# Performance work log

Measured on AMD Instinct MI355X. Metric: run time of the kernel, lower is better.

The kernel has to match this reference:

```python
import jax, jax.numpy as jnp
import numpy as np

NUM_WIRES = 20
DEPTH = 4


def setup_inputs() -> dict:
    key = jax.random.key(0)
    x = jax.random.normal(key, (NUM_WIRES,), dtype=jnp.float32)
    return {"x": x}


def _apply_1q(state, gate, wire):
    # state: flat [2^n] complex; apply 2x2 gate on `wire`
    s = state.reshape(2 ** wire, 2, -1)
    return jnp.einsum('ab,ibj->iaj', gate, s).reshape(-1)


def _apply_cnot(state, control):
    # CNOT on adjacent wires (control, control+1): flip target where control==1
    s = state.reshape(2 ** control, 2, 2, -1)
    s = jnp.concatenate([s[:, :1], s[:, 1:, ::-1]], axis=1)
    return s.reshape(-1)


def _simulate(x):
    n = NUM_WIRES
    state = jnp.zeros(2 ** n, dtype=jnp.complex64).at[0].set(1.0)
    half = (x.astype(jnp.float32) * 0.5)
    c = jnp.cos(half).astype(jnp.complex64)  # [n]
    s = jnp.sin(half).astype(jnp.complex64)  # [n]
    for _ in range(DEPTH):
        for w in range(n):
            cw, sw = c[w], s[w]
            rx = jnp.stack([jnp.stack([cw, -1j * sw]), jnp.stack([-1j * sw, cw])])
            ry = jnp.stack([jnp.stack([cw, -sw]), jnp.stack([sw, cw])])
            state = _apply_1q(state, rx, w)
            state = _apply_1q(state, ry, w)
        for w in range(n - 1):
            state = _apply_cnot(state, w)
    probs = jnp.abs(state) ** 2  # real float32 [2^n]
    expz = []
    for i in range(n):
        p = probs.reshape(2 ** i, 2, -1).sum(axis=(0, 2))
        expz.append(p[0] - p[1])
    return jnp.stack(expz).astype(jnp.float32)  # [n] <Z_i>


def reference(x):
    return _simulate(x)
```

## Files before the change

kernel.cpp:

```cpp
#include <hip/hip_runtime.h>


#define NW 20

__device__ __forceinline__ float2 cmul(float2 a, float2 b) {
    return make_float2(a.x*b.x - a.y*b.y, a.x*b.y + a.y*b.x);
}

__device__ __forceinline__ void apply_gate(float2& a0, float2& a1,
                                           float2 u00, float2 u01,
                                           float2 u10, float2 u11) {
    float2 b0, b1;
    b0.x = u00.x*a0.x - u00.y*a0.y + u01.x*a1.x - u01.y*a1.y;
    b0.y = u00.x*a0.y + u00.y*a0.x + u01.x*a1.y + u01.y*a1.x;
    b1.x = u10.x*a0.x - u10.y*a0.y + u11.x*a1.x - u11.y*a1.y;
    b1.y = u10.x*a0.y + u10.y*a0.x + u11.x*a1.y + u11.y*a1.x;
    a0 = b0; a1 = b1;
}

__device__ __forceinline__ float2 shflx(float2 v, int m) {
    float2 r;
    r.x = __shfl_xor(v.x, m, 64);
    r.y = __shfl_xor(v.y, m, 64);
    return r;
}

template<int A>
__device__ __forceinline__ void gate_regbit(float2 (&amp)[8], const float2* __restrict__ Gw) {
    float2 u00 = Gw[0], u01 = Gw[1], u10 = Gw[2], u11 = Gw[3];
    #pragma unroll
    for (int r = 0; r < 8; r++)
        if (!(r & (1 << A)))
            apply_gate(amp[r], amp[r | (1 << A)], u00, u01, u10, u11);
}

template<int A, int LM>
__device__ __forceinline__ void swap_reg_lane(float2 (&amp)[8], unsigned lane) {
    bool hb = (lane & (unsigned)LM) != 0u;
    #pragma unroll
    for (int r = 0; r < 8; r++) {
        if (!(r & (1 << A))) {
            float2 lo = amp[r], hi = amp[r | (1 << A)];
            float2 xs = hb ? lo : hi;
            float2 ys = shflx(xs, LM);
            amp[r]            = hb ? ys : lo;
            amp[r | (1 << A)] = hb ? hi : ys;
        }
    }
}

__global__ void prep_gates(const float* __restrict__ x, float2* __restrict__ G) {
    int w = threadIdx.x;
    if (w < NW) {
        float h = 0.5f * x[w];
        float c = cosf(h), s = sinf(h);
        float cc = c*c, ss = s*s, cs = c*s;
        G[w*4+0] = make_float2(cc,  ss);
        G[w*4+1] = make_float2(-cs, -cs);
        G[w*4+2] = make_float2(cs,  -cs);
        G[w*4+3] = make_float2(cc,  -ss);
    }
}

template<int MODE>
__global__ __launch_bounds__(512) void stageA(const float2* __restrict__ src,
                                              float2* __restrict__ dst,
                                              const float2* __restrict__ G) {
    __shared__ float2 lds[4096];
    const unsigned t = threadIdx.x;
    const unsigned lane = t & 63u, wv = t >> 6;
    const unsigned H   = blockIdx.x;
    const unsigned Hp  = H ^ (H >> 1);
    const unsigned inj = (H & 1u) << 11;
    const unsigned lb  = (wv << 9) | (lane << 3);
    const unsigned gb  = (lb ^ (lb >> 1)) ^ inj;

    float2 amp[8];
    if (MODE == 1) {
        const float4* q = (const float4*)(src + ((size_t)Hp << 12) + (gb & ~7u));
        float4 q0 = q[0], q1 = q[1], q2 = q[2], q3 = q[3];
        float2 e0 = make_float2(q0.x,q0.y), e1 = make_float2(q0.z,q0.w);
        float2 e2 = make_float2(q1.x,q1.y), e3 = make_float2(q1.z,q1.w);
        float2 e4 = make_float2(q2.x,q2.y), e5 = make_float2(q2.z,q2.w);
        float2 e6 = make_float2(q3.x,q3.y), e7 = make_float2(q3.z,q3.w);
        bool f = (gb & 4u) != 0u;
        amp[0] = f ? e4 : e0;  amp[1] = f ? e5 : e1;
        amp[2] = f ? e7 : e3;  amp[3] = f ? e6 : e2;
        amp[4] = f ? e2 : e6;  amp[5] = f ? e3 : e7;
        amp[6] = f ? e1 : e5;  amp[7] = f ? e0 : e4;
    } else {
        float2 P = make_float2(1.0f, 0.0f);
        #pragma unroll
        for (int b = 12; b <= 19; b++)
            P = cmul(P, G[(19-b)*4 + (int)((Hp >> (b-12)) & 1u)*2]);
        #pragma unroll
        for (int b = 3; b <= 11; b++)
            P = cmul(P, G[(19-b)*4 + (int)((gb >> b) & 1u)*2]);
        float2 Tt[8];
        #pragma unroll
        for (int j = 0; j < 8; j++) {
            float2 v = cmul(G[18*4 + ((j>>1)&1)*2], G[19*4 + (j&1)*2]);
            v = cmul(G[17*4 + ((j>>2)&1)*2], v);
            Tt[j] = cmul(P, v);
        }
        bool f = (gb & 4u) != 0u;
        amp[0] = f ? Tt[4] : Tt[0];  amp[1] = f ? Tt[5] : Tt[1];
        amp[2] = f ? Tt[7] : Tt[3];  amp[3] = f ? Tt[6] : Tt[2];
        amp[4] = f ? Tt[2] : Tt[6];  amp[5] = f ? Tt[3] : Tt[7];
        amp[6] = f ? Tt[1] : Tt[5];  amp[7] = f ? Tt[0] : Tt[4];
    }

    gate_regbit<0>(amp, G + 19*4);
    gate_regbit<1>(amp, G + 18*4);
    gate_regbit<2>(amp, G + 17*4);
    swap_reg_lane<0,1>(amp, lane);
    swap_reg_lane<1,2>(amp, lane);
    swap_reg_lane<2,4>(amp, lane);
    gate_regbit<0>(amp, G + 16*4);
    gate_regbit<1>(amp, G + 15*4);
    gate_regbit<2>(amp, G + 14*4);
    swap_reg_lane<0,8>(amp, lane);
    swap_reg_lane<1,16>(amp, lane);
    swap_reg_lane<2,32>(amp, lane);
    gate_regbit<0>(amp, G + 13*4);
    gate_regbit<1>(amp, G + 12*4);
    gate_regbit<2>(amp, G + 11*4);
    #pragma unroll
    for (int k = 0; k < 8; k++) lds[(wv << 9) | ((unsigned)k << 6) | lane] = amp[k];
    __syncthreads();
    #pragma unroll
    for (int k = 0; k < 8; k++) amp[k] = lds[((unsigned)k << 9) | (wv << 6) | lane];
    gate_regbit<0>(amp, G + 10*4);
    gate_regbit<1>(amp, G +  9*4);
    gate_regbit<2>(amp, G +  8*4);
    float2* d = dst + ((size_t)H << 12);
    #pragma unroll
    for (int k = 0; k < 8; k++) d[((unsigned)k << 9) | (wv << 6) | lane] = amp[k];
}

template<int FUSE>
__global__ __launch_bounds__(512) void stageB(float2* __restrict__ st,
                                              const float2* __restrict__ G,
                                              float* __restrict__ partial) {
    __shared__ float2 lds[4096];
    const unsigned t = threadIdx.x, lane = t & 63u, wv = t >> 6;
    const unsigned bb = blockIdx.x;
    const unsigned m = lane & 15u, l45 = lane >> 4;

    float2 amp[8];
    #pragma unroll
    for (int k = 0; k < 8; k++) {
        unsigned h = (unsigned)k | (l45 << 3) | (wv << 5);
        amp[k] = st[((size_t)h << 12) | (bb << 4) | m];
    }
    gate_regbit<0>(amp, G + 7*4);
    gate_regbit<1>(amp, G + 6*4);
    gate_regbit<2>(amp, G + 5*4);
    swap_reg_lane<0,16>(amp, lane);
    swap_reg_lane<1,32>(amp, lane);
    gate_regbit<0>(amp, G + 4*4);
    gate_regbit<1>(amp, G + 3*4);
    #pragma unroll
    for (int k = 0; k < 8; k++) {
        unsigned li = lane | ((((unsigned)k >> 2) & 1u) << 6) | (((unsigned)k & 1u) << 7)
                    | ((((unsigned)k >> 1) & 1u) << 8) | (wv << 9);
        lds[li] = amp[k];
    }
    __syncthreads();
    #pragma unroll
    for (int k = 0; k < 8; k++) amp[k] = lds[lane | (wv << 6) | ((unsigned)k << 9)];
    gate_regbit<0>(amp, G + 2*4);
    gate_regbit<1>(amp, G + 1*4);
    gate_regbit<2>(amp, G + 0*4);

    if (!FUSE) {
        #pragma unroll
        for (int k = 0; k < 8; k++) {
            unsigned h = l45 | (wv << 2) | ((unsigned)k << 5);
            st[((size_t)h << 12) | (bb << 4) | m] = amp[k];
        }
    } else {
        float p[8];
        #pragma unroll
        for (int k = 0; k < 8; k++) p[k] = amp[k].x*amp[k].x + amp[k].y*amp[k].y;
        float Se = p[0]+p[3]+p[5]+p[6];
        float So = p[1]+p[2]+p[4]+p[7];
        float D  = Se - So;
        float S0 = (p[0]+p[1]+p[2]+p[3]) - (p[4]+p[5]+p[6]+p[7]);
        float S1 = (p[0]+p[1]+p[6]+p[7]) - (p[2]+p[3]+p[4]+p[5]);
        unsigned hlow = l45 | (wv << 2);
        unsigned v = (hlow << 12) | (bb << 4) | m;
        unsigned cm = v; cm ^= cm >> 1; cm ^= cm >> 2; cm ^= cm >> 4;
        cm ^= cm >> 8; cm ^= cm >> 16;
        float acc[NW];
        acc[0] = S0; acc[1] = S1; acc[2] = D;
        #pragma unroll
        for (int w = 3; w < NW; w++)
            acc[w] = ((cm >> (19 - w)) & 1u) ? -D : D;

        __syncthreads();
        float* red = (float*)lds;
        #pragma unroll
        for (int w = 0; w < NW; w++) {
            float s = acc[w];
            #pragma unroll
            for (int off = 32; off; off >>= 1) s += __shfl_down(s, off, 64);
            if (lane == 0) red[wv*NW + w] = s;
        }
        __syncthreads();
        if (t < NW) {
            float s = 0.0f;
            #pragma unroll
            for (int w8 = 0; w8 < 8; w8++) s += red[w8*NW + (int)t];
            partial[bb*NW + t] = s;
        }
    }
}

__global__ __launch_bounds__(256) void reduce_out(const float* __restrict__ partial,
                                                  float* __restrict__ out) {
    __shared__ float red[4*NW];
    unsigned t = threadIdx.x;
    float vals[NW];
    #pragma unroll
    for (int w = 0; w < NW; w++) vals[w] = partial[t*NW + w];
    #pragma unroll
    for (int w = 0; w < NW; w++) {
        float v = vals[w];
        #pragma unroll
        for (int off = 32; off; off >>= 1) v += __shfl_down(v, off, 64);
        if ((t & 63u) == 0u) red[(t >> 6)*NW + w] = v;
    }
    __syncthreads();
    if (t < NW) out[t] = red[t] + red[NW+t] + red[2*NW+t] + red[3*NW+t];
}

extern "C" void kernel_launch(void* const* d_in, const int* in_sizes, int n_in,
                              void* d_out, int out_size, void* d_ws, size_t ws_size,
                              hipStream_t stream) {
    (void)in_sizes; (void)n_in; (void)out_size; (void)ws_size;
    const float* x = (const float*)d_in[0];
    float* out = (float*)d_out;

    char* ws = (char*)d_ws;
    float2* gates   = (float2*)ws;
    float*  partial = (float*)(ws + 1024);
    float2* buf0    = (float2*)(ws + 65536);
    float2* buf1    = (float2*)(ws + 65536 + (size_t)(8u << 20));

    prep_gates<<<1, 32, 0, stream>>>(x, gates);
    stageA<0><<<256, 512, 0, stream>>>(buf1 , buf0, gates);
    stageB<0><<<256, 512, 0, stream>>>(buf0, gates, nullptr);
    stageA<1><<<256, 512, 0, stream>>>(buf0, buf1, gates);
    stageB<0><<<256, 512, 0, stream>>>(buf1, gates, nullptr);
    stageA<1><<<256, 512, 0, stream>>>(buf1, buf0, gates);
    stageB<1><<<256, 512, 0, stream>>>(buf0, gates, partial);
    reduce_out<<<1, 256, 0, stream>>>(partial, out);
}
```

Baseline: 72.75 us.

## Repartition qubit stages into 512 blocks of 256 threads with 11/9 bit split

Changes the work split from 256 blocks of 4096 amplitudes to 512 blocks of 2048 amplitudes. Stage A now handles wires 9-19 and stage B handles wires 0-8, with new global and LDS index mappings and lane swaps. The partial-sum reduction is adjusted for 512 partials. The goal is more blocks across the MI355X's many CUs to improve occupancy and load balance. The cost is more complex, possibly less coalesced global access in stage B, where each contiguous run is only 4 elements.

```diff
diff --git a/kernel.cpp b/kernel.cpp
--- a/kernel.cpp
+++ b/kernel.cpp
@@ -63,21 +63,21 @@
 }
 
 template<int MODE>
-__global__ __launch_bounds__(512) void stageA(const float2* __restrict__ src,
+__global__ __launch_bounds__(256) void stageA(const float2* __restrict__ src,
                                               float2* __restrict__ dst,
                                               const float2* __restrict__ G) {
-    __shared__ float2 lds[4096];
+    __shared__ float2 lds[2048];
     const unsigned t = threadIdx.x;
     const unsigned lane = t & 63u, wv = t >> 6;
-    const unsigned H   = blockIdx.x;
-    const unsigned Hp  = H ^ (H >> 1);
-    const unsigned inj = (H & 1u) << 11;
+    const unsigned Hf  = blockIdx.x;
+    const unsigned Hp  = Hf ^ (Hf >> 1);
+    const unsigned inj = (Hf & 1u) << 10;
     const unsigned lb  = (wv << 9) | (lane << 3);
     const unsigned gb  = (lb ^ (lb >> 1)) ^ inj;
 
     float2 amp[8];
     if (MODE == 1) {
-        const float4* q = (const float4*)(src + ((size_t)Hp << 12) + (gb & ~7u));
+        const float4* q = (const float4*)(src + ((size_t)Hp << 11) + (gb & ~7u));
         float4 q0 = q[0], q1 = q[1], q2 = q[2], q3 = q[3];
         float2 e0 = make_float2(q0.x,q0.y), e1 = make_float2(q0.z,q0.w);
         float2 e2 = make_float2(q1.x,q1.y), e3 = make_float2(q1.z,q1.w);
@@ -91,10 +91,10 @@
     } else {
         float2 P = make_float2(1.0f, 0.0f);
         #pragma unroll
-        for (int b = 12; b <= 19; b++)
-            P = cmul(P, G[(19-b)*4 + (int)((Hp >> (b-12)) & 1u)*2]);
-        #pragma unroll
-        for (int b = 3; b <= 11; b++)
+        for (int b = 11; b <= 19; b++)
+            P = cmul(P, G[(19-b)*4 + (int)((Hp >> (b-11)) & 1u)*2]);
+        #pragma unroll
+        for (int b = 3; b <= 10; b++)
             P = cmul(P, G[(19-b)*4 + (int)((gb >> b) & 1u)*2]);
         float2 Tt[8];
         #pragma unroll
@@ -126,49 +126,53 @@
     gate_regbit<1>(amp, G + 12*4);
     gate_regbit<2>(amp, G + 11*4);
     #pragma unroll
-    for (int k = 0; k < 8; k++) lds[(wv << 9) | ((unsigned)k << 6) | lane] = amp[k];
+    for (int k = 0; k < 8; k++) lds[lane | ((unsigned)k << 6) | (wv << 9)] = amp[k];
     __syncthreads();
     #pragma unroll
-    for (int k = 0; k < 8; k++) amp[k] = lds[((unsigned)k << 9) | (wv << 6) | lane];
-    gate_regbit<0>(amp, G + 10*4);
-    gate_regbit<1>(amp, G +  9*4);
-    gate_regbit<2>(amp, G +  8*4);
-    float2* d = dst + ((size_t)H << 12);
-    #pragma unroll
-    for (int k = 0; k < 8; k++) d[((unsigned)k << 9) | (wv << 6) | lane] = amp[k];
+    for (int k = 0; k < 8; k++)
+        amp[k] = lds[lane | (((unsigned)k & 1u) << 6) | (wv << 7) | (((unsigned)k >> 1) << 9)];
+    gate_regbit<1>(amp, G + 10*4);
+    gate_regbit<2>(amp, G +  9*4);
+    float2* d = dst + ((size_t)Hf << 11);
+    #pragma unroll
+    for (int k = 0; k < 8; k++)
+        d[lane | (((unsigned)k & 1u) << 6) | (wv << 7) | (((unsigned)k >> 1) << 9)] = amp[k];
 }
 
 template<int FUSE>
-__global__ __launch_bounds__(512) void stageB(float2* __restrict__ st,
+__global__ __launch_bounds__(256) void stageB(float2* __restrict__ st,
                                               const float2* __restrict__ G,
                                               float* __restrict__ partial) {
-    __shared__ float2 lds[4096];
+    __shared__ float2 lds[2048];
     const unsigned t = threadIdx.x, lane = t & 63u, wv = t >> 6;
     const unsigned bb = blockIdx.x;
-    const unsigned m = lane & 15u, l45 = lane >> 4;
+    const unsigned l01 = lane & 3u, l2345 = (lane >> 2) & 15u;
 
     float2 amp[8];
     #pragma unroll
     for (int k = 0; k < 8; k++) {
-        unsigned h = (unsigned)k | (l45 << 3) | (wv << 5);
-        amp[k] = st[((size_t)h << 12) | (bb << 4) | m];
-    }
-    gate_regbit<0>(amp, G + 7*4);
-    gate_regbit<1>(amp, G + 6*4);
-    gate_regbit<2>(amp, G + 5*4);
-    swap_reg_lane<0,16>(amp, lane);
-    swap_reg_lane<1,32>(amp, lane);
-    gate_regbit<0>(amp, G + 4*4);
-    gate_regbit<1>(amp, G + 3*4);
+        unsigned idx = l01 | (bb << 2) | ((unsigned)k << 11) | (l2345 << 14) | (wv << 18);
+        amp[k] = st[idx];
+    }
+    gate_regbit<0>(amp, G + 8*4);
+    gate_regbit<1>(amp, G + 7*4);
+    gate_regbit<2>(amp, G + 6*4);
+    swap_reg_lane<0,4>(amp, lane);
+    swap_reg_lane<1,8>(amp, lane);
+    swap_reg_lane<2,16>(amp, lane);
+    gate_regbit<0>(amp, G + 5*4);
+    gate_regbit<1>(amp, G + 4*4);
+    gate_regbit<2>(amp, G + 3*4);
+    #pragma unroll
+    for (int k = 0; k < 8; k++) lds[lane | ((unsigned)k << 6) | (wv << 9)] = amp[k];
+    __syncthreads();
     #pragma unroll
     for (int k = 0; k < 8; k++) {
-        unsigned li = lane | ((((unsigned)k >> 2) & 1u) << 6) | (((unsigned)k & 1u) << 7)
-                    | ((((unsigned)k >> 1) & 1u) << 8) | (wv << 9);
-        lds[li] = amp[k];
-    }
-    __syncthreads();
-    #pragma unroll
-    for (int k = 0; k < 8; k++) amp[k] = lds[lane | (wv << 6) | ((unsigned)k << 9)];
+        unsigned a = (lane & 31u) | (((unsigned)k & 1u) << 5) | (((lane >> 5) & 1u) << 6)
+                   | ((wv & 1u) << 7) | (((wv >> 1) & 1u) << 8)
+                   | ((((unsigned)k >> 1) & 1u) << 9) | ((((unsigned)k >> 2) & 1u) << 10);
+        amp[k] = lds[a];
+    }
     gate_regbit<0>(amp, G + 2*4);
     gate_regbit<1>(amp, G + 1*4);
     gate_regbit<2>(amp, G + 0*4);
@@ -176,8 +180,11 @@
     if (!FUSE) {
         #pragma unroll
         for (int k = 0; k < 8; k++) {
-            unsigned h = l45 | (wv << 2) | ((unsigned)k << 5);
-            st[((size_t)h << 12) | (bb << 4) | m] = amp[k];
+            unsigned idx = (lane & 3u) | (bb << 2) | (((lane >> 2) & 7u) << 11)
+                         | (((lane >> 5) & 1u) << 14) | (wv << 15)
+                         | (((unsigned)k & 1u) << 17) | ((((unsigned)k >> 1) & 1u) << 18)
+                         | ((((unsigned)k >> 2) & 1u) << 19);
+            st[idx] = amp[k];
         }
     } else {
         float p[8];
@@ -188,8 +195,8 @@
         float D  = Se - So;
         float S0 = (p[0]+p[1]+p[2]+p[3]) - (p[4]+p[5]+p[6]+p[7]);
         float S1 = (p[0]+p[1]+p[6]+p[7]) - (p[2]+p[3]+p[4]+p[5]);
-        unsigned hlow = l45 | (wv << 2);
-        unsigned v = (hlow << 12) | (bb << 4) | m;
+        unsigned v = (lane & 3u) | (bb << 2) | (((lane >> 2) & 7u) << 11)
+                   | (((lane >> 5) & 1u) << 14) | (wv << 15);
         unsigned cm = v; cm ^= cm >> 1; cm ^= cm >> 2; cm ^= cm >> 4;
         cm ^= cm >> 8; cm ^= cm >> 16;
         float acc[NW];
@@ -211,15 +218,15 @@
         if (t < NW) {
             float s = 0.0f;
             #pragma unroll
-            for (int w8 = 0; w8 < 8; w8++) s += red[w8*NW + (int)t];
+            for (int w4 = 0; w4 < 4; w4++) s += red[w4*NW + (int)t];
             partial[bb*NW + t] = s;
         }
     }
 }
 
-__global__ __launch_bounds__(256) void reduce_out(const float* __restrict__ partial,
+__global__ __launch_bounds__(512) void reduce_out(const float* __restrict__ partial,
                                                   float* __restrict__ out) {
-    __shared__ float red[4*NW];
+    __shared__ float red[8*NW];
     unsigned t = threadIdx.x;
     float vals[NW];
     #pragma unroll
@@ -232,7 +239,12 @@
         if ((t & 63u) == 0u) red[(t >> 6)*NW + w] = v;
     }
     __syncthreads();
-    if (t < NW) out[t] = red[t] + red[NW+t] + red[2*NW+t] + red[3*NW+t];
+    if (t < NW) {
+        float s = 0.0f;
+        #pragma unroll
+        for (int w8 = 0; w8 < 8; w8++) s += red[w8*NW + (int)t];
+        out[t] = s;
+    }
 }
 
 extern "C" void kernel_launch(void* const* d_in, const int* in_sizes, int n_in,
@@ -249,11 +261,11 @@
     float2* buf1    = (float2*)(ws + 65536 + (size_t)(8u << 20));
 
     prep_gates<<<1, 32, 0, stream>>>(x, gates);
-    stageA<0><<<256, 512, 0, stream>>>(buf1 , buf0, gates);
-    stageB<0><<<256, 512, 0, stream>>>(buf0, gates, nullptr);
-    stageA<1><<<256, 512, 0, stream>>>(buf0, buf1, gates);
-    stageB<0><<<256, 512, 0, stream>>>(buf1, gates, nullptr);
-    stageA<1><<<256, 512, 0, stream>>>(buf1, buf0, gates);
-    stageB<1><<<256, 512, 0, stream>>>(buf0, gates, partial);
-    reduce_out<<<1, 256, 0, stream>>>(partial, out);
-}
+    stageA<0><<<512, 256, 0, stream>>>(buf1 , buf0, gates);
+    stageB<0><<<512, 256, 0, stream>>>(buf0, gates, nullptr);
+    stageA<1><<<512, 256, 0, stream>>>(buf0, buf1, gates);
+    stageB<0><<<512, 256, 0, stream>>>(buf1, gates, nullptr);
+    stageA<1><<<512, 256, 0, stream>>>(buf1, buf0, gates);
+    stageB<1><<<512, 256, 0, stream>>>(buf0, gates, partial);
+    reduce_out<<<1, 512, 0, stream>>>(partial, out);
+}
```

New measurement: 90.93 us. +25.0%, slower.

## Fuse CNOT-ladder-aware gate layers into four state passes instead of six

Applied to the files above, without the earlier changes.

Restructures the simulation so that each global-memory pass over the 2^20 state applies gates from more than one circuit layer. It does this by tracking the CNOT ladder as a parity (prefix-XOR) relabelling, applied through new gate_mreg and gate_mlane helpers that choose operand order per element. This cuts the number of full state read/write sweeps, which dominate kernel time, and drops two launches. In exchange it adds extra LDS transposes, barriers, shuffles and bit-twiddling per pass, plus substantial correctness risk in the index mappings.

```diff
diff --git a/kernel.cpp b/kernel.cpp
--- a/kernel.cpp
+++ b/kernel.cpp
@@ -5,16 +5,18 @@
 
 __device__ __forceinline__ float2 cmul(float2 a, float2 b) {
     return make_float2(a.x*b.x - a.y*b.y, a.x*b.y + a.y*b.x);
+}
+
+__device__ __forceinline__ float2 rowmul(float2 u, float2 a, float2 v, float2 b) {
+    return make_float2(u.x*a.x - u.y*a.y + v.x*b.x - v.y*b.y,
+                       u.x*a.y + u.y*a.x + v.x*b.y + v.y*b.x);
 }
 
 __device__ __forceinline__ void apply_gate(float2& a0, float2& a1,
                                            float2 u00, float2 u01,
                                            float2 u10, float2 u11) {
-    float2 b0, b1;
-    b0.x = u00.x*a0.x - u00.y*a0.y + u01.x*a1.x - u01.y*a1.y;
-    b0.y = u00.x*a0.y + u00.y*a0.x + u01.x*a1.y + u01.y*a1.x;
-    b1.x = u10.x*a0.x - u10.y*a0.y + u11.x*a1.x - u11.y*a1.y;
-    b1.y = u10.x*a0.y + u10.y*a0.x + u11.x*a1.y + u11.y*a1.x;
+    float2 b0 = rowmul(u00, a0, u01, a1);
+    float2 b1 = rowmul(u10, a0, u11, a1);
     a0 = b0; a1 = b1;
 }
 
@@ -23,6 +25,13 @@
     r.x = __shfl_xor(v.x, m, 64);
     r.y = __shfl_xor(v.y, m, 64);
     return r;
+}
+
+__device__ __forceinline__ unsigned sfx(unsigned x) {
+    x ^= x >> 1; x ^= x >> 2; x ^= x >> 4; x ^= x >> 8; x ^= x >> 16; return x;
+}
+__device__ __forceinline__ unsigned pfx2(unsigned x) {
+    x ^= x >> 2; x ^= x >> 4; x ^= x >> 8; x ^= x >> 16; return x;
 }
 
 template<int A>
@@ -46,6 +55,34 @@
             amp[r]            = hb ? ys : lo;
             amp[r | (1 << A)] = hb ? hi : ys;
         }
+    }
+}
+
+template<int M, int SEL, int RH>
+__device__ __forceinline__ void gate_mreg(float2 (&amp)[8], const float2* __restrict__ Gw,
+                                          unsigned Rk) {
+    float2 u00 = Gw[0], u01 = Gw[1], u10 = Gw[2], u11 = Gw[3];
+    #pragma unroll
+    for (int r = 0; r < 8; r++) {
+        if (r & SEL) continue;
+        int rp = r ^ M;
+        unsigned fl = (Rk + (unsigned)__popc((unsigned)r & (unsigned)RH)) & 1u;
+        if (fl == 0u) apply_gate(amp[r], amp[rp], u00, u01, u10, u11);
+        else          apply_gate(amp[rp], amp[r], u00, u01, u10, u11);
+    }
+}
+
+template<int LM, int RH>
+__device__ __forceinline__ void gate_mlane(float2 (&amp)[8], const float2* __restrict__ Gw,
+                                           unsigned myzb, unsigned Rk) {
+    float2 u00 = Gw[0], u01 = Gw[1], u10 = Gw[2], u11 = Gw[3];
+    #pragma unroll
+    for (int r = 0; r < 8; r++) {
+        float2 part = shflx(amp[r], LM);
+        unsigned fl = (Rk + (unsigned)__popc((unsigned)r & (unsigned)RH)) & 1u;
+        float2 mine = amp[r];
+        amp[r] = ((myzb ^ fl) == 0u) ? rowmul(u00, mine, u01, part)
+                                     : rowmul(u10, part, u11, mine);
     }
 }
 
@@ -62,9 +99,7 @@
     }
 }
 
-template<int MODE>
-__global__ __launch_bounds__(512) void stageA(const float2* __restrict__ src,
-                                              float2* __restrict__ dst,
+__global__ __launch_bounds__(512) void passA1(float2* __restrict__ dst,
                                               const float2* __restrict__ G) {
     __shared__ float2 lds[4096];
     const unsigned t = threadIdx.x;
@@ -76,19 +111,7 @@
     const unsigned gb  = (lb ^ (lb >> 1)) ^ inj;
 
     float2 amp[8];
-    if (MODE == 1) {
-        const float4* q = (const float4*)(src + ((size_t)Hp << 12) + (gb & ~7u));
-        float4 q0 = q[0], q1 = q[1], q2 = q[2], q3 = q[3];
-        float2 e0 = make_float2(q0.x,q0.y), e1 = make_float2(q0.z,q0.w);
-        float2 e2 = make_float2(q1.x,q1.y), e3 = make_float2(q1.z,q1.w);
-        float2 e4 = make_float2(q2.x,q2.y), e5 = make_float2(q2.z,q2.w);
-        float2 e6 = make_float2(q3.x,q3.y), e7 = make_float2(q3.z,q3.w);
-        bool f = (gb & 4u) != 0u;
-        amp[0] = f ? e4 : e0;  amp[1] = f ? e5 : e1;
-        amp[2] = f ? e7 : e3;  amp[3] = f ? e6 : e2;
-        amp[4] = f ? e2 : e6;  amp[5] = f ? e3 : e7;
-        amp[6] = f ? e1 : e5;  amp[7] = f ? e0 : e4;
-    } else {
+    {
         float2 P = make_float2(1.0f, 0.0f);
         #pragma unroll
         for (int b = 12; b <= 19; b++)
@@ -109,7 +132,6 @@
         amp[4] = f ? Tt[2] : Tt[6];  amp[5] = f ? Tt[3] : Tt[7];
         amp[6] = f ? Tt[1] : Tt[5];  amp[7] = f ? Tt[0] : Tt[4];
     }
-
     gate_regbit<0>(amp, G + 19*4);
     gate_regbit<1>(amp, G + 18*4);
     gate_regbit<2>(amp, G + 17*4);
@@ -138,82 +160,283 @@
     for (int k = 0; k < 8; k++) d[((unsigned)k << 9) | (wv << 6) | lane] = amp[k];
 }
 
-template<int FUSE>
-__global__ __launch_bounds__(512) void stageB(float2* __restrict__ st,
+__global__ __launch_bounds__(512) void passB2(float2* __restrict__ st,
+                                              const float2* __restrict__ G) {
+    __shared__ float2 lds[4096];
+    const unsigned t = threadIdx.x, lane = t & 63u, wv = t >> 6;
+    const unsigned bb = blockIdx.x;
+    const unsigned l012 = lane & 7u;
+    const unsigned l3 = (lane >> 3) & 1u, l4 = (lane >> 4) & 1u, l5 = (lane >> 5) & 1u;
+    const unsigned w0 = wv & 1u, w1 = (wv >> 1) & 1u, w2 = (wv >> 2) & 1u;
+
+    float2 amp[8];
+    const unsigned base = l012 | (bb << 3) | (w0 << 11) | (l3 << 15) | (l4 << 16)
+                        | (l5 << 17) | (w1 << 18) | (w2 << 19);
+    #pragma unroll
+    for (int k = 0; k < 8; k++)
+        amp[k] = st[base | ((unsigned)(k & 1) << 12) | ((unsigned)((k >> 1) & 1) << 13)
+                         | ((unsigned)(k >> 2) << 14)];
+
+    gate_regbit<0>(amp, G + 7*4);
+    gate_regbit<1>(amp, G + 6*4);
+    gate_regbit<2>(amp, G + 5*4);
+    swap_reg_lane<0, 8>(amp, lane);
+    swap_reg_lane<1,16>(amp, lane);
+    swap_reg_lane<2,32>(amp, lane);
+    gate_regbit<0>(amp, G + 4*4);
+    gate_regbit<1>(amp, G + 3*4);
+    gate_regbit<2>(amp, G + 2*4);
+    #pragma unroll
+    for (int k = 0; k < 8; k++) lds[lane | ((unsigned)k << 6) | (wv << 9)] = amp[k];
+    __syncthreads();
+    #pragma unroll
+    for (int k = 0; k < 8; k++)
+        amp[k] = lds[lane | (w0 << 6) | (w1 << 7) | (w2 << 8)
+                     | ((unsigned)((k >> 2) & 1) << 9) | ((unsigned)(k & 1) << 10)
+                     | ((unsigned)((k >> 1) & 1) << 11)];
+    __syncthreads();
+    gate_regbit<0>(amp, G + 1*4);
+    gate_regbit<1>(amp, G + 0*4);
+    {
+        unsigned zk = l012 | (bb << 3) | (l3 << 12) | (l4 << 13) | (l5 << 14)
+                    | (w0 << 15) | (w1 << 16) | (w2 << 17);
+        unsigned T = sfx(zk);
+        gate_mlane<1, 7>(amp, G + 19*4, lane & 1u,        (T >> 1) & 1u);
+        gate_mlane<3, 7>(amp, G + 18*4, (lane >> 1) & 1u, (T >> 2) & 1u);
+        gate_mlane<6, 7>(amp, G + 17*4, (lane >> 2) & 1u, (T >> 3) & 1u);
+        gate_mlane<24, 3>(amp, G + 6*4, l4, (T >> 14) & 1u);
+        gate_mlane<48, 3>(amp, G + 5*4, l5, (T >> 15) & 1u);
+        gate_mreg<3, 2, 0>(amp, G + 0*4, 0u);
+    }
+    #pragma unroll
+    for (int k = 0; k < 8; k++) lds[lane | ((unsigned)k << 6) | (wv << 9)] = amp[k];
+    __syncthreads();
+    #pragma unroll
+    for (int k = 0; k < 8; k++)
+        amp[k] = lds[l012 | (w0 << 3) | (w1 << 4) | ((unsigned)(k & 1) << 5)
+                     | (l4 << 6) | (w2 << 7) | (l5 << 8)
+                     | ((unsigned)((k >> 1) & 1) << 9) | ((unsigned)(k >> 2) << 10)
+                     | (l3 << 11)];
+    __syncthreads();
+    {
+        unsigned zk2 = l012 | (bb << 3) | (l3 << 17) | (l4 << 18) | (l5 << 11)
+                     | (w0 << 12) | (w1 << 13) | (w2 << 19);
+        unsigned T2 = sfx(zk2);
+        gate_mreg<3, 2, 4>(amp, G + 4*4, (T2 >> 16) & 1u);
+        gate_mreg<6, 4, 0>(amp, G + 3*4, (T2 >> 17) & 1u);
+        gate_mlane<24, 0>(amp, G + 1*4, l4, (T2 >> 19) & 1u);
+    }
+    #pragma unroll
+    for (int k = 0; k < 8; k++) lds[lane | ((unsigned)k << 6) | (wv << 9)] = amp[k];
+    __syncthreads();
+    #pragma unroll
+    for (int k = 0; k < 8; k++)
+        amp[k] = lds[l012 | (l4 << 3) | (w1 << 4) | ((unsigned)(k & 1) << 5)
+                     | (l5 << 6) | (w0 << 7) | (l3 << 8)
+                     | ((unsigned)((k >> 1) & 1) << 9) | ((unsigned)(k >> 2) << 10)
+                     | (w2 << 11)];
+    {
+        unsigned zk3 = l012 | (bb << 3) | (l3 << 16) | (l4 << 17) | (l5 << 14)
+                     | (w0 << 15) | (w1 << 18) | (w2 << 19);
+        unsigned T3 = sfx(zk3);
+        gate_mreg<3, 2, 4>(amp, G + 7*4, (T3 >> 13) & 1u);
+        gate_mlane<24, 0>(amp, G + 2*4, l4, (T3 >> 18) & 1u);
+    }
+    const unsigned sb = l012 | (bb << 3) | (l5 << 14) | (w0 << 15) | (l3 << 16)
+                      | (l4 << 17) | (w1 << 18) | (w2 << 19);
+    #pragma unroll
+    for (int k = 0; k < 8; k++)
+        st[sb | ((unsigned)(k & 1) << 11) | ((unsigned)((k >> 1) & 1) << 12)
+              | ((unsigned)(k >> 2) << 13)] = amp[k];
+}
+
+__global__ __launch_bounds__(512) void passA3(const float2* __restrict__ src,
+                                              float2* __restrict__ dst,
+                                              const float2* __restrict__ G) {
+    __shared__ float2 lds[4096];
+    const unsigned t = threadIdx.x, lane = t & 63u, wv = t >> 6;
+    const unsigned H   = blockIdx.x;
+    const unsigned Hp  = H ^ (H >> 1);
+    const unsigned inj = (H & 1u) << 11;
+    const unsigned lb  = (wv << 9) | (lane << 3);
+    const unsigned gb  = (lb ^ (lb >> 1)) ^ inj;
+
+    float2 amp[8];
+    {
+        const float4* q = (const float4*)(src + ((size_t)Hp << 12) + (gb & ~7u));
+        float4 q0 = q[0], q1 = q[1], q2 = q[2], q3 = q[3];
+        float2 e0 = make_float2(q0.x,q0.y), e1 = make_float2(q0.z,q0.w);
+        float2 e2 = make_float2(q1.x,q1.y), e3 = make_float2(q1.z,q1.w);
+        float2 e4 = make_float2(q2.x,q2.y), e5 = make_float2(q2.z,q2.w);
+        float2 e6 = make_float2(q3.x,q3.y), e7 = make_float2(q3.z,q3.w);
+        bool f = (gb & 4u) != 0u;
+        amp[0] = f ? e4 : e0;  amp[1] = f ? e5 : e1;
+        amp[2] = f ? e7 : e3;  amp[3] = f ? e6 : e2;
+        amp[4] = f ? e2 : e6;  amp[5] = f ? e3 : e7;
+        amp[6] = f ? e1 : e5;  amp[7] = f ? e0 : e4;
+    }
+    swap_reg_lane<0,1>(amp, lane);
+    swap_reg_lane<1,2>(amp, lane);
+    swap_reg_lane<2,4>(amp, lane);
+    gate_regbit<0>(amp, G + 16*4);
+    gate_regbit<1>(amp, G + 15*4);
+    gate_regbit<2>(amp, G + 14*4);
+    swap_reg_lane<0,8>(amp, lane);
+    swap_reg_lane<1,16>(amp, lane);
+    swap_reg_lane<2,32>(amp, lane);
+    gate_regbit<0>(amp, G + 13*4);
+    gate_regbit<1>(amp, G + 12*4);
+    gate_regbit<2>(amp, G + 11*4);
+    #pragma unroll
+    for (int k = 0; k < 8; k++) lds[lane | ((unsigned)k << 6) | (wv << 9)] = amp[k];
+    __syncthreads();
+    #pragma unroll
+    for (int k = 0; k < 8; k++) amp[k] = lds[lane | (wv << 6) | ((unsigned)k << 9)];
+    __syncthreads();
+    gate_regbit<0>(amp, G + 10*4);
+    gate_regbit<1>(amp, G +  9*4);
+    gate_regbit<2>(amp, G +  8*4);
+    {
+        unsigned zk = lane | (wv << 6) | (H << 12);
+        unsigned T = sfx(zk);
+        gate_mlane<1, 7>(amp, G + 19*4, lane & 1u,        (T >> 1) & 1u);
+        gate_mlane<3, 7>(amp, G + 18*4, (lane >> 1) & 1u, (T >> 2) & 1u);
+        gate_mlane<6, 7>(amp, G + 17*4, (lane >> 2) & 1u, (T >> 3) & 1u);
+        gate_mlane<12, 7>(amp, G + 16*4, (lane >> 3) & 1u, (T >> 4) & 1u);
+        gate_mlane<24, 7>(amp, G + 15*4, (lane >> 4) & 1u, (T >> 5) & 1u);
+        gate_mlane<48, 7>(amp, G + 14*4, (lane >> 5) & 1u, (T >> 6) & 1u);
+        gate_mreg<3, 2, 4>(amp, G + 9*4, (T >> 11) & 1u);
+        gate_mreg<6, 4, 0>(amp, G + 8*4, (T >> 12) & 1u);
+    }
+    #pragma unroll
+    for (int k = 0; k < 8; k++) lds[lane | (wv << 6) | ((unsigned)k << 9)] = amp[k];
+    __syncthreads();
+    const unsigned l3v = (lane >> 3) & 1u, l4v = (lane >> 4) & 1u, l5v = (lane >> 5) & 1u;
+    const unsigned w0v = wv & 1u, w1v = (wv >> 1) & 1u, w2v = (wv >> 2) & 1u;
+    #pragma unroll
+    for (int k = 0; k < 8; k++)
+        amp[k] = lds[(lane & 7u) | (l5v << 3) | (w0v << 4)
+                     | ((unsigned)(k & 1) << 5) | ((unsigned)((k >> 1) & 1) << 6)
+                     | ((unsigned)(k >> 2) << 7)
+                     | (l3v << 8) | (l4v << 9) | (w1v << 10) | (w2v << 11)];
+    {
+        unsigned zkB = (lane & 7u) | (l5v << 3) | (w0v << 4) | (l3v << 8) | (l4v << 9)
+                     | (w1v << 10) | (w2v << 11) | (H << 12);
+        unsigned TB = sfx(zkB);
+        gate_mreg<3, 2, 4>(amp, G + 13*4, (TB >> 7) & 1u);
+        gate_mreg<6, 4, 0>(amp, G + 12*4, (TB >> 8) & 1u);
+    }
+    swap_reg_lane<0, 8>(amp, lane);
+    {
+        unsigned zkC = (lane & 7u) | (l5v << 3) | (w0v << 4) | (l3v << 5) | (l4v << 9)
+                     | (w1v << 10) | (w2v << 11) | (H << 12);
+        unsigned TC = sfx(zkC);
+        gate_mreg<5, 1, 0>(amp, G + 11*4, (TC >> 9) & 1u);
+    }
+    swap_reg_lane<1, 16>(amp, lane);
+    {
+        unsigned zkD = (lane & 7u) | (l5v << 3) | (w0v << 4) | (l3v << 5) | (l4v << 6)
+                     | (w1v << 10) | (w2v << 11) | (H << 12);
+        unsigned TD = sfx(zkD);
+        gate_mreg<3, 2, 0>(amp, G + 10*4, (TD >> 10) & 1u);
+    }
+    const unsigned sb = (lane & 7u) | (l5v << 3) | (w0v << 4) | (l3v << 5) | (l4v << 6)
+                      | (w1v << 10) | (w2v << 11) | (H << 12);
+    #pragma unroll
+    for (int k = 0; k < 8; k++)
+        dst[sb | ((unsigned)((k >> 2) & 1) << 7) | ((unsigned)(k & 1) << 8)
+              | ((unsigned)((k >> 1) & 1) << 9)] = amp[k];
+}
+
+__global__ __launch_bounds__(512) void passB4(const float2* __restrict__ st,
                                               const float2* __restrict__ G,
                                               float* __restrict__ partial) {
     __shared__ float2 lds[4096];
     const unsigned t = threadIdx.x, lane = t & 63u, wv = t >> 6;
     const unsigned bb = blockIdx.x;
-    const unsigned m = lane & 15u, l45 = lane >> 4;
+    const unsigned l012 = lane & 7u;
+    const unsigned l3 = (lane >> 3) & 1u, l4 = (lane >> 4) & 1u, l5 = (lane >> 5) & 1u;
+    const unsigned w0 = wv & 1u, w1 = (wv >> 1) & 1u, w2 = (wv >> 2) & 1u;
 
     float2 amp[8];
-    #pragma unroll
-    for (int k = 0; k < 8; k++) {
-        unsigned h = (unsigned)k | (l45 << 3) | (wv << 5);
-        amp[k] = st[((size_t)h << 12) | (bb << 4) | m];
-    }
-    gate_regbit<0>(amp, G + 7*4);
-    gate_regbit<1>(amp, G + 6*4);
-    gate_regbit<2>(amp, G + 5*4);
-    swap_reg_lane<0,16>(amp, lane);
-    swap_reg_lane<1,32>(amp, lane);
-    gate_regbit<0>(amp, G + 4*4);
-    gate_regbit<1>(amp, G + 3*4);
-    #pragma unroll
-    for (int k = 0; k < 8; k++) {
-        unsigned li = lane | ((((unsigned)k >> 2) & 1u) << 6) | (((unsigned)k & 1u) << 7)
-                    | ((((unsigned)k >> 1) & 1u) << 8) | (wv << 9);
-        lds[li] = amp[k];
-    }
-    __syncthreads();
-    #pragma unroll
-    for (int k = 0; k < 8; k++) amp[k] = lds[lane | (wv << 6) | ((unsigned)k << 9)];
-    gate_regbit<0>(amp, G + 2*4);
-    gate_regbit<1>(amp, G + 1*4);
-    gate_regbit<2>(amp, G + 0*4);
-
-    if (!FUSE) {
-        #pragma unroll
-        for (int k = 0; k < 8; k++) {
-            unsigned h = l45 | (wv << 2) | ((unsigned)k << 5);
-            st[((size_t)h << 12) | (bb << 4) | m] = amp[k];
-        }
-    } else {
-        float p[8];
-        #pragma unroll
-        for (int k = 0; k < 8; k++) p[k] = amp[k].x*amp[k].x + amp[k].y*amp[k].y;
-        float Se = p[0]+p[3]+p[5]+p[6];
-        float So = p[1]+p[2]+p[4]+p[7];
-        float D  = Se - So;
-        float S0 = (p[0]+p[1]+p[2]+p[3]) - (p[4]+p[5]+p[6]+p[7]);
-        float S1 = (p[0]+p[1]+p[6]+p[7]) - (p[2]+p[3]+p[4]+p[5]);
-        unsigned hlow = l45 | (wv << 2);
-        unsigned v = (hlow << 12) | (bb << 4) | m;
-        unsigned cm = v; cm ^= cm >> 1; cm ^= cm >> 2; cm ^= cm >> 4;
-        cm ^= cm >> 8; cm ^= cm >> 16;
-        float acc[NW];
-        acc[0] = S0; acc[1] = S1; acc[2] = D;
-        #pragma unroll
-        for (int w = 3; w < NW; w++)
-            acc[w] = ((cm >> (19 - w)) & 1u) ? -D : D;
-
-        __syncthreads();
-        float* red = (float*)lds;
-        #pragma unroll
-        for (int w = 0; w < NW; w++) {
-            float s = acc[w];
-            #pragma unroll
-            for (int off = 32; off; off >>= 1) s += __shfl_down(s, off, 64);
-            if (lane == 0) red[wv*NW + w] = s;
-        }
-        __syncthreads();
-        if (t < NW) {
-            float s = 0.0f;
-            #pragma unroll
-            for (int w8 = 0; w8 < 8; w8++) s += red[w8*NW + (int)t];
-            partial[bb*NW + t] = s;
-        }
+    const unsigned base = l012 | (bb << 3) | (w0 << 11) | (l3 << 15) | (l4 << 16)
+                        | (l5 << 17) | (w1 << 18) | (w2 << 19);
+    #pragma unroll
+    for (int k = 0; k < 8; k++)
+        amp[k] = st[base | ((unsigned)(k & 1) << 12) | ((unsigned)((k >> 1) & 1) << 13)
+                         | ((unsigned)(k >> 2) << 14)];
+    {
+        unsigned T = sfx(base);
+        gate_mreg<3, 2, 4>(amp, G + 6*4, (T >> 14) & 1u);
+        gate_mreg<6, 4, 0>(amp, G + 5*4, (T >> 15) & 1u);
+    }
+    swap_reg_lane<0, 8>(amp, lane);
+    {
+        unsigned zkB = l012 | (bb << 3) | (w0 << 11) | (l3 << 12) | (l4 << 16)
+                     | (l5 << 17) | (w1 << 18) | (w2 << 19);
+        unsigned TB = sfx(zkB);
+        gate_mreg<5, 1, 0>(amp, G + 4*4, (TB >> 16) & 1u);
+    }
+    swap_reg_lane<1, 16>(amp, lane);
+    {
+        unsigned zkC = l012 | (bb << 3) | (w0 << 11) | (l3 << 12) | (l4 << 13)
+                     | (l5 << 17) | (w1 << 18) | (w2 << 19);
+        unsigned TC = sfx(zkC);
+        gate_mreg<3, 2, 0>(amp, G + 3*4, (TC >> 17) & 1u);
+    }
+    swap_reg_lane<2, 32>(amp, lane);
+    {
+        unsigned zkD = l012 | (bb << 3) | (w0 << 11) | (l3 << 12) | (l4 << 13)
+                     | (l5 << 14) | (w1 << 18) | (w2 << 19);
+        unsigned TD = sfx(zkD);
+        gate_mreg<6, 4, 0>(amp, G + 2*4, (TD >> 18) & 1u);
+    }
+    #pragma unroll
+    for (int k = 0; k < 8; k++) lds[lane | ((unsigned)k << 6) | (wv << 9)] = amp[k];
+    __syncthreads();
+    #pragma unroll
+    for (int k = 0; k < 8; k++)
+        amp[k] = lds[l012 | (l4 << 3) | (l5 << 4) | (w0 << 5) | (w1 << 6) | (w2 << 7)
+                     | ((unsigned)(k & 1) << 8) | (l3 << 9)
+                     | ((unsigned)((k >> 1) & 1) << 10) | ((unsigned)(k >> 2) << 11)];
+    const unsigned zkE = l012 | (bb << 3) | (l3 << 11) | (l4 << 12) | (l5 << 13)
+                       | (w0 << 14) | (w1 << 15) | (w2 << 16);
+    {
+        unsigned TE = sfx(zkE);
+        gate_mreg<3, 2, 4>(amp, G + 1*4, 0u);
+        gate_mreg<6, 4, 0>(amp, G + 0*4, 0u);
+        gate_mlane<24, 7>(amp, G + 7*4, l4, (TE >> 13) & 1u);
+    }
+    float p[8];
+    #pragma unroll
+    for (int r = 0; r < 8; r++) p[r] = amp[r].x*amp[r].x + amp[r].y*amp[r].y;
+    float E   = (p[0]+p[1]+p[4]+p[5]) - (p[2]+p[3]+p[6]+p[7]);
+    float Do  = (p[0]+p[2]+p[5]+p[7]) - (p[1]+p[3]+p[4]+p[6]);
+    float S19 = (p[0]+p[1]+p[2]+p[3]) - (p[4]+p[5]+p[6]+p[7]);
+    unsigned t2 = pfx2(zkE);
+    float acc[NW];
+    acc[0] = S19;
+    #pragma unroll
+    for (int w = 1; w < NW; w++) {
+        int b = 19 - w;
+        float v = (b & 1) ? Do : E;
+        acc[w] = ((t2 >> b) & 1u) ? -v : v;
+    }
+    __syncthreads();
+    float* red = (float*)lds;
+    #pragma unroll
+    for (int w = 0; w < NW; w++) {
+        float s = acc[w];
+        #pragma unroll
+        for (int off = 32; off; off >>= 1) s += __shfl_down(s, off, 64);
+        if (lane == 0) red[wv*NW + w] = s;
+    }
+    __syncthreads();
+    if (t < NW) {
+        float s = 0.0f;
+        #pragma unroll
+        for (int v8 = 0; v8 < 8; v8++) s += red[v8*NW + (int)t];
+        partial[bb*NW + t] = s;
     }
 }
 
@@ -249,11 +472,9 @@
     float2* buf1    = (float2*)(ws + 65536 + (size_t)(8u << 20));
 
     prep_gates<<<1, 32, 0, stream>>>(x, gates);
-    stageA<0><<<256, 512, 0, stream>>>(buf1 , buf0, gates);
-    stageB<0><<<256, 512, 0, stream>>>(buf0, gates, nullptr);
-    stageA<1><<<256, 512, 0, stream>>>(buf0, buf1, gates);
-    stageB<0><<<256, 512, 0, stream>>>(buf1, gates, nullptr);
-    stageA<1><<<256, 512, 0, stream>>>(buf1, buf0, gates);
-    stageB<1><<<256, 512, 0, stream>>>(buf0, gates, partial);
+    passA1<<<256, 512, 0, stream>>>(buf0, gates);
+    passB2<<<256, 512, 0, stream>>>(buf0, gates);
+    passA3<<<256, 512, 0, stream>>>(buf0, buf1, gates);
+    passB4<<<256, 512, 0, stream>>>(buf1, gates, partial);
     reduce_out<<<1, 256, 0, stream>>>(partial, out);
 }
```

Measured after the change: 87.39 us. 1.2x slower.

## Fuse all stages into one cooperative persistent kernel with grid syncs

Applied to the files above, without the earlier changes.

Replaces eight separate kernel launches (gate prep, six stage kernels, final reduce) with a single cooperative kernel that uses grid.sync between phases. Gate matrices are computed per block into shared memory instead of a separate kernel writing to global memory. This targets launch overhead and inter-kernel gaps. The cost is grid-wide barriers, extra block-level syncs added for shared-memory reuse, and loss of __restrict__ hints on the gate pointers.

```diff
diff --git a/kernel.cpp b/kernel.cpp
--- a/kernel.cpp
+++ b/kernel.cpp
@@ -1,4 +1,7 @@
 #include <hip/hip_runtime.h>
+#include <hip/hip_cooperative_groups.h>
+
+namespace cg = cooperative_groups;
 
 
 #define NW 20
@@ -26,7 +29,7 @@
 }
 
 template<int A>
-__device__ __forceinline__ void gate_regbit(float2 (&amp)[8], const float2* __restrict__ Gw) {
+__device__ __forceinline__ void gate_regbit(float2 (&amp)[8], const float2* Gw) {
     float2 u00 = Gw[0], u01 = Gw[1], u10 = Gw[2], u11 = Gw[3];
     #pragma unroll
     for (int r = 0; r < 8; r++)
@@ -49,24 +52,8 @@
     }
 }
 
-__global__ void prep_gates(const float* __restrict__ x, float2* __restrict__ G) {
-    int w = threadIdx.x;
-    if (w < NW) {
-        float h = 0.5f * x[w];
-        float c = cosf(h), s = sinf(h);
-        float cc = c*c, ss = s*s, cs = c*s;
-        G[w*4+0] = make_float2(cc,  ss);
-        G[w*4+1] = make_float2(-cs, -cs);
-        G[w*4+2] = make_float2(cs,  -cs);
-        G[w*4+3] = make_float2(cc,  -ss);
-    }
-}
-
 template<int MODE>
-__global__ __launch_bounds__(512) void stageA(const float2* __restrict__ src,
-                                              float2* __restrict__ dst,
-                                              const float2* __restrict__ G) {
-    __shared__ float2 lds[4096];
+__device__ void phaseA(float2* lds, const float2* src, float2* dst, const float2* G) {
     const unsigned t = threadIdx.x;
     const unsigned lane = t & 63u, wv = t >> 6;
     const unsigned H   = blockIdx.x;
@@ -130,6 +117,7 @@
     __syncthreads();
     #pragma unroll
     for (int k = 0; k < 8; k++) amp[k] = lds[((unsigned)k << 9) | (wv << 6) | lane];
+    __syncthreads();
     gate_regbit<0>(amp, G + 10*4);
     gate_regbit<1>(amp, G +  9*4);
     gate_regbit<2>(amp, G +  8*4);
@@ -139,10 +127,7 @@
 }
 
 template<int FUSE>
-__global__ __launch_bounds__(512) void stageB(float2* __restrict__ st,
-                                              const float2* __restrict__ G,
-                                              float* __restrict__ partial) {
-    __shared__ float2 lds[4096];
+__device__ void phaseB(float2* lds, float2* st, const float2* G, float* partial) {
     const unsigned t = threadIdx.x, lane = t & 63u, wv = t >> 6;
     const unsigned bb = blockIdx.x;
     const unsigned m = lane & 15u, l45 = lane >> 4;
@@ -169,6 +154,7 @@
     __syncthreads();
     #pragma unroll
     for (int k = 0; k < 8; k++) amp[k] = lds[lane | (wv << 6) | ((unsigned)k << 9)];
+    __syncthreads();
     gate_regbit<0>(amp, G + 2*4);
     gate_regbit<1>(amp, G + 1*4);
     gate_regbit<2>(amp, G + 0*4);
@@ -198,7 +184,6 @@
         for (int w = 3; w < NW; w++)
             acc[w] = ((cm >> (19 - w)) & 1u) ? -D : D;
 
-        __syncthreads();
         float* red = (float*)lds;
         #pragma unroll
         for (int w = 0; w < NW; w++) {
@@ -217,22 +202,63 @@
     }
 }
 
-__global__ __launch_bounds__(256) void reduce_out(const float* __restrict__ partial,
-                                                  float* __restrict__ out) {
-    __shared__ float red[4*NW];
-    unsigned t = threadIdx.x;
-    float vals[NW];
-    #pragma unroll
-    for (int w = 0; w < NW; w++) vals[w] = partial[t*NW + w];
-    #pragma unroll
-    for (int w = 0; w < NW; w++) {
-        float v = vals[w];
-        #pragma unroll
-        for (int off = 32; off; off >>= 1) v += __shfl_down(v, off, 64);
-        if ((t & 63u) == 0u) red[(t >> 6)*NW + w] = v;
-    }
-    __syncthreads();
-    if (t < NW) out[t] = red[t] + red[NW+t] + red[2*NW+t] + red[3*NW+t];
+__global__ __launch_bounds__(512) void qfm_all(const float* __restrict__ x,
+                                               float2* __restrict__ buf0,
+                                               float2* __restrict__ buf1,
+                                               float* __restrict__ partial,
+                                               float* __restrict__ out) {
+    __shared__ float2 lds[4096];
+    __shared__ float2 Gs[4*NW];
+    const unsigned t = threadIdx.x;
+
+    if (t < NW) {
+        float h = 0.5f * x[t];
+        float c = cosf(h), s = sinf(h);
+        float cc = c*c, ss = s*s, cs = c*s;
+        Gs[t*4+0] = make_float2(cc,  ss);
+        Gs[t*4+1] = make_float2(-cs, -cs);
+        Gs[t*4+2] = make_float2(cs,  -cs);
+        Gs[t*4+3] = make_float2(cc,  -ss);
+    }
+    __syncthreads();
+
+    cg::grid_group grid = cg::this_grid();
+
+    phaseA<0>(lds, buf1, buf0, Gs);
+    grid.sync();
+    phaseB<0>(lds, buf0, Gs, nullptr);
+    grid.sync();
+    phaseA<1>(lds, buf0, buf1, Gs);
+    grid.sync();
+    phaseB<0>(lds, buf1, Gs, nullptr);
+    grid.sync();
+    phaseA<1>(lds, buf1, buf0, Gs);
+    grid.sync();
+    phaseB<1>(lds, buf0, Gs, partial);
+    grid.sync();
+
+    if (blockIdx.x == 0) {
+        float vals[NW];
+        #pragma unroll
+        for (int w = 0; w < NW; w++)
+            vals[w] = (t < 256u) ? partial[t*NW + w] : 0.0f;
+        float* red = (float*)lds;
+        const unsigned lane = t & 63u, wv = t >> 6;
+        #pragma unroll
+        for (int w = 0; w < NW; w++) {
+            float v = vals[w];
+            #pragma unroll
+            for (int off = 32; off; off >>= 1) v += __shfl_down(v, off, 64);
+            if (lane == 0) red[wv*NW + w] = v;
+        }
+        __syncthreads();
+        if (t < NW) {
+            float s = 0.0f;
+            #pragma unroll
+            for (int w8 = 0; w8 < 8; w8++) s += red[w8*NW + (int)t];
+            out[t] = s;
+        }
+    }
 }
 
 extern "C" void kernel_launch(void* const* d_in, const int* in_sizes, int n_in,
@@ -243,17 +269,11 @@
     float* out = (float*)d_out;
 
     char* ws = (char*)d_ws;
-    float2* gates   = (float2*)ws;
     float*  partial = (float*)(ws + 1024);
     float2* buf0    = (float2*)(ws + 65536);
     float2* buf1    = (float2*)(ws + 65536 + (size_t)(8u << 20));
 
-    prep_gates<<<1, 32, 0, stream>>>(x, gates);
-    stageA<0><<<256, 512, 0, stream>>>(buf1 , buf0, gates);
-    stageB<0><<<256, 512, 0, stream>>>(buf0, gates, nullptr);
-    stageA<1><<<256, 512, 0, stream>>>(buf0, buf1, gates);
-    stageB<0><<<256, 512, 0, stream>>>(buf1, gates, nullptr);
-    stageA<1><<<256, 512, 0, stream>>>(buf1, buf0, gates);
-    stageB<1><<<256, 512, 0, stream>>>(buf0, gates, partial);
-    reduce_out<<<1, 256, 0, stream>>>(partial, out);
-}
+    void* args[] = { (void*)&x, (void*)&buf0, (void*)&buf1, (void*)&partial, (void*)&out };
+    hipLaunchCooperativeKernel((const void*)qfm_all, dim3(256), dim3(512),
+                               args, 0, stream);
+}
```

Result: slower. 243.8 us (+235.1%).
